# Optimization experiments

Hardware: AMD Instinct MI355X
Metric: run time of the kernel (lower is better)

Reference implementation:

```python
import jax, jax.numpy as jnp
import numpy as np

TAU = 2.0          # LIFNode tau
ALPHA = 2.0        # spikingjelly ATan surrogate alpha (default)
EPS = 1e-5         # nn.LayerNorm eps
SCALE = 0.125      # qk_scale
NUM_HEADS = 2

@jax.custom_vjp
def spike(x):
    # heaviside(x >= 0) with ATan surrogate gradient
    return (x >= 0.0).astype(x.dtype)

def _spike_fwd(x):
    return spike(x), x

def _spike_bwd(x, g):
    sg = (ALPHA / 2.0) / (1.0 + (jnp.pi / 2.0 * ALPHA * x) ** 2)
    return (g * sg,)

spike.defvjp(_spike_fwd, _spike_bwd)

def lif(x, v_th):
    # LIFNode(tau=2.0, decay_input=True, v_reset=0.0, detach_reset=True)
    # x: [T, ...]; sequential membrane-potential scan over T
    def step(v, xt):
        v = v + (xt - v) / TAU                      # charge with input decay
        s = spike(v - v_th)                          # fire
        v = v * (1.0 - jax.lax.stop_gradient(s))     # hard reset to 0, detached
        return v, s
    _, s = jax.lax.scan(step, jnp.zeros_like(x[0]), x)
    return s

def ln(x, w, b):
    m = x.mean(-1, keepdims=True)
    var = x.var(-1, keepdims=True)
    return (x - m) / jnp.sqrt(var + EPS) * w + b

def setup_inputs() -> dict:
    key = jax.random.key(0)
    ks = jax.random.split(key, 6)
    T, B, L, H = 4, 64, 200, 256
    x = jax.random.normal(ks[0], (T, B, L, H), dtype=jnp.float32)
    std = 0.05
    qw = jax.random.normal(ks[1], (H, H), dtype=jnp.float32) * std
    kw = jax.random.normal(ks[2], (H, H), dtype=jnp.float32) * std
    vw = jax.random.normal(ks[3], (H, H), dtype=jnp.float32) * std
    pw = jax.random.normal(ks[4], (H, H), dtype=jnp.float32) * std
    pb = jnp.zeros((H,), dtype=jnp.float32)
    ones = jnp.ones((H,), dtype=jnp.float32)
    zeros = jnp.zeros((H,), dtype=jnp.float32)
    return {
        'x': x,
        'qw': qw, 'q_ln_w': ones, 'q_ln_b': zeros,
        'kw': kw, 'k_ln_w': ones, 'k_ln_b': zeros,
        'vw': vw, 'v_ln_w': ones, 'v_ln_b': zeros,
        'pw': pw, 'pb': pb, 'p_ln_w': ones, 'p_ln_b': zeros,
    }

def reference(x, qw, q_ln_w, q_ln_b, kw, k_ln_w, k_ln_b, vw, v_ln_w, v_ln_b, pw, pb, p_ln_w, p_ln_b):
    T, B, L, H = x.shape
    nh = NUM_HEADS
    dh = H // nh

    def branch(w, lw, lb):
        y = ln(x @ w.T, lw, lb)           # Linear (no bias) -> LayerNorm
        y = lif(y, 1.0)                   # LIF spikes in {0,1}
        return y.reshape(T, B, L, nh, dh).transpose(0, 1, 3, 2, 4)  # [T,B,h,L,dh]

    q = branch(qw, q_ln_w, q_ln_b)
    k = branch(kw, k_ln_w, k_ln_b)
    v = branch(vw, v_ln_w, v_ln_b)

    attn = jnp.einsum('tbhld,tbhmd->tbhlm', q, k) * SCALE   # [T,B,h,L,L]
    y = jnp.einsum('tbhlm,tbhmd->tbhld', attn, v)            # [T,B,h,L,dh]
    y = y.transpose(0, 1, 3, 2, 4).reshape(T, B, L, H)
    y = lif(y, 0.5)                                          # attn_lif, v_threshold=0.5
    y = ln(y @ pw.T + pb, p_ln_w, p_ln_b)                    # proj Linear (bias) -> LN
    return lif(y, 1.0)                                       # proj_lif
```

## Files before the change

kernel.cpp:

```cpp
#include <hip/hip_runtime.h>

#define T_ 4
#define B_ 64
#define L_ 200
#define H_ 256
#define NH_ 2
#define DH_ 128
#define LCAP 12800

typedef short short8_t __attribute__((ext_vector_type(8)));
typedef float f32x4 __attribute__((ext_vector_type(4)));

#define MFMA_BF16(a, b, c) __builtin_amdgcn_mfma_f32_16x16x32_bf16((a), (b), (c), 0, 0, 0)

__device__ __forceinline__ unsigned short bf16rn(float f) {
  unsigned u = __float_as_uint(f);
  return (unsigned short)((u + 0x7FFFu + ((u >> 16) & 1u)) >> 16);
}
__device__ __forceinline__ float bf16tof(unsigned short h) {
  return __uint_as_float(((unsigned)h) << 16);
}

__device__ __forceinline__ short8_t unpack_bf16(uint2 v) {
  union { short8_t s; unsigned u[4]; } r;
  r.u[0] = __builtin_amdgcn_perm(0u, v.x, 0x0C010C00u) * 0x3F80u;
  r.u[1] = __builtin_amdgcn_perm(0u, v.x, 0x0C030C02u) * 0x3F80u;
  r.u[2] = __builtin_amdgcn_perm(0u, v.y, 0x0C010C00u) * 0x3F80u;
  r.u[3] = __builtin_amdgcn_perm(0u, v.y, 0x0C030C02u) * 0x3F80u;
  return r.s;
}

__global__ void pack_w(const float* __restrict__ qw, const float* __restrict__ kw,
                       const float* __restrict__ vw, const float* __restrict__ pw,
                       short* __restrict__ wf, float* __restrict__ wT) {
  int id = blockIdx.x * 256 + threadIdx.x;
  if (id < 262144) {
    int mat = id >> 16, k = (id >> 8) & 255, j = id & 255;
    const float* src = (mat == 0) ? qw : (mat == 1) ? kw : (mat == 2) ? vw : pw;
    wT[id] = src[j * 256 + k];
  }
  int fid = id - 262144;
  if (fid >= 0 && fid < 98304) {
    int lane = fid & 63, kc = (fid >> 6) & 7, nt = (fid >> 9) & 15, ms = fid >> 13;
    int mat = ms / 3, s = ms - mat * 3;
    const float* src = (mat == 0) ? qw : (mat == 1) ? kw : (mat == 2) ? vw : pw;
    int n = nt * 16 + (lane & 15), q = lane >> 4;
    for (int j = 0; j < 8; j++) {
      float v = src[n * 256 + kc * 32 + q * 8 + j];
      unsigned short h1 = bf16rn(v);
      float r1 = v - bf16tof(h1);
      unsigned short h2 = bf16rn(r1);
      float r2 = r1 - bf16tof(h2);
      unsigned short h3 = bf16rn(r2);
      wf[fid * 8 + j] = (short)((s == 0) ? h1 : (s == 1) ? h2 : h3);
    }
  }
}

__global__ void zero_cnt(int* __restrict__ cnt) {
  if (threadIdx.x < 4) cnt[threadIdx.x] = 0;
}

#define QKV_STEP(kc, b0a, b1a)                                                  \
  do {                                                                          \
    int ap_ = (lane ^ (kc)) * 8;                                                \
    short8_t a0_[2], a1_[2];                                                    \
    a0_[0] = *(const short8_t*)&sa[(kc) * 512 + ap_];                           \
    a0_[1] = *(const short8_t*)&sa[(8 + (kc)) * 512 + ap_];                     \
    a1_[0] = *(const short8_t*)&sa[8192 + (kc) * 512 + ap_];                    \
    a1_[1] = *(const short8_t*)&sa[8192 + (8 + (kc)) * 512 + ap_];              \
    _Pragma("unroll")                                                           \
    for (int jj_ = 0; jj_ < 4; jj_++) {                                         \
      _Pragma("unroll")                                                         \
      for (int mt_ = 0; mt_ < 2; mt_++) {                                       \
        hi[mt_][jj_] = MFMA_BF16(a0_[mt_], b0a[jj_], hi[mt_][jj_]);             \
        lo[mt_][jj_] = MFMA_BF16(a0_[mt_], b1a[jj_], lo[mt_][jj_]);             \
        lo[mt_][jj_] = MFMA_BF16(a1_[mt_], b0a[jj_], lo[mt_][jj_]);             \
        lo[mt_][jj_] = MFMA_BF16(a1_[mt_], b1a[jj_], lo[mt_][jj_]);             \
      }                                                                         \
    }                                                                           \
  } while (0)

__global__ __launch_bounds__(256, 2)
void gemm_qkv(const float* __restrict__ xf, const short* __restrict__ wf,
              const float* __restrict__ qlnw, const float* __restrict__ qlnb,
              const float* __restrict__ klnw, const float* __restrict__ klnb,
              const float* __restrict__ vlnw, const float* __restrict__ vlnb,
              unsigned char* __restrict__ Qsp, unsigned char* __restrict__ Ksp,
              unsigned char* __restrict__ Vsp,
              int* __restrict__ cnt, int* __restrict__ list) {
  __shared__ short sa[2 * 8192];
  __shared__ float reds[32][4];
  __shared__ float redq[32][4];
  __shared__ int pf[24];
  const int tid = threadIdx.x;
  const int w = tid >> 6, lane = tid & 63;
  const int q = lane >> 4, ln = lane & 15;
  const int p0 = blockIdx.x * 8;
  const int jbase = w * 4;

  if (tid < 24) pf[tid] = 0;

  short8_t bA0[4], bA1[4], bB0[4], bB1[4];
#pragma unroll
  for (int jj = 0; jj < 4; jj++) {
    const short* bp = wf + (size_t)(jbase + jj) * 4096 + lane * 8;
    bA0[jj] = *(const short8_t*)bp;
    bA1[jj] = *(const short8_t*)(bp + 65536);
  }

  for (int it = 0; it < 4; it++) {
    int cid = tid + 256 * it;
    int r = cid >> 5, ck = cid & 31;
    int k0 = ck * 8, kc = ck >> 2, cq = ck & 3;
    int mt = r >> 4, m = r & 15;
    int p = r >> 2, t = r & 3;
    int pi = p0 + p;
    int b = pi / L_, l = pi % L_;
    size_t nrow = ((size_t)t * B_ + b) * L_ + l;
    int base = ((mt * 8 + kc) * 512) + (((cq * 16 + m) ^ (kc & 7)) * 8);
    float4 v0 = *(const float4*)(xf + nrow * H_ + k0);
    float4 v1 = *(const float4*)(xf + nrow * H_ + k0 + 4);
    float f[8] = {v0.x, v0.y, v0.z, v0.w, v1.x, v1.y, v1.z, v1.w};
    union { short8_t v; short s[8]; } H1, H2;
#pragma unroll
    for (int e = 0; e < 8; e++) {
      unsigned short h1 = bf16rn(f[e]);
      float r1 = f[e] - bf16tof(h1);
      unsigned short h2 = bf16rn(r1);
      H1.s[e] = (short)h1; H2.s[e] = (short)h2;
    }
    *(short8_t*)&sa[base] = H1.v;
    *(short8_t*)&sa[base + 8192] = H2.v;
  }
  __syncthreads();

  for (int mat = 0; mat < 3; mat++) {
    const float* lnw = (mat == 0) ? qlnw : (mat == 1) ? klnw : vlnw;
    const float* lnb = (mat == 0) ? qlnb : (mat == 1) ? klnb : vlnb;
    unsigned char* spk = (mat == 0) ? Qsp : (mat == 1) ? Ksp : Vsp;
    const short* wb = wf + (size_t)mat * 196608;

    f32x4 hi[2][4], lo[2][4];
#pragma unroll
    for (int mt = 0; mt < 2; mt++)
#pragma unroll
      for (int jj = 0; jj < 4; jj++) {
        f32x4 z = {0.f, 0.f, 0.f, 0.f};
        hi[mt][jj] = z; lo[mt][jj] = z;
      }

#pragma unroll
    for (int kh = 0; kh < 4; kh++) {
      const int kc = 2 * kh;
#pragma unroll
      for (int jj = 0; jj < 4; jj++) {
        const short* bp = wb + (size_t)(kc + 1) * 512 + (size_t)(jbase + jj) * 4096 + lane * 8;
        bB0[jj] = *(const short8_t*)bp;
        bB1[jj] = *(const short8_t*)(bp + 65536);
      }
      QKV_STEP(kc, bA0, bA1);
      if (kc + 2 < 8 || mat < 2) {
        const short* nx = (kc + 2 < 8) ? (wb + (size_t)(kc + 2) * 512) : (wb + 196608);
#pragma unroll
        for (int jj = 0; jj < 4; jj++) {
          const short* bp = nx + (size_t)(jbase + jj) * 4096 + lane * 8;
          bA0[jj] = *(const short8_t*)bp;
          bA1[jj] = *(const short8_t*)(bp + 65536);
        }
      }
      QKV_STEP(kc + 1, bB0, bB1);
    }

    float y[2][4][4];
#pragma unroll
    for (int mt = 0; mt < 2; mt++)
#pragma unroll
      for (int jj = 0; jj < 4; jj++)
#pragma unroll
        for (int i = 0; i < 4; i++)
          y[mt][jj][i] = hi[mt][jj][i] + lo[mt][jj][i];

#pragma unroll
    for (int mt = 0; mt < 2; mt++)
#pragma unroll
      for (int i = 0; i < 4; i++) {
        float s = y[mt][0][i] + y[mt][1][i] + y[mt][2][i] + y[mt][3][i];
        float ss = y[mt][0][i] * y[mt][0][i] + y[mt][1][i] * y[mt][1][i]
                 + y[mt][2][i] * y[mt][2][i] + y[mt][3][i] * y[mt][3][i];
#pragma unroll
        for (int o = 1; o < 16; o <<= 1) {
          s += __shfl_xor(s, o, 64);
          ss += __shfl_xor(ss, o, 64);
        }
        if (ln == 0) { reds[16 * mt + 4 * q + i][w] = s; redq[16 * mt + 4 * q + i][w] = ss; }
      }
    __syncthreads();
    float m_[2][4], rs_[2][4], tolr[2][4];
#pragma unroll
    for (int mt = 0; mt < 2; mt++)
#pragma unroll
      for (int i = 0; i < 4; i++) {
        int r = 16 * mt + 4 * q + i;
        float S = reds[r][0] + reds[r][1] + reds[r][2] + reds[r][3];
        float Q2 = redq[r][0] + redq[r][1] + redq[r][2] + redq[r][3];
        float mm = S * (1.0f / 256.0f);
        float var = Q2 * (1.0f / 256.0f) - mm * mm;
        float rs = 1.0f / sqrtf(var + 1e-5f);
        m_[mt][i] = mm; rs_[mt][i] = rs;
        tolr[mt][i] = 1.5e-4f + 3e-6f * (4.0f + fabsf(mm) * rs);
      }

    int fl[2] = {0, 0};
#pragma unroll
    for (int mt = 0; mt < 2; mt++) {
      int pi = p0 + 4 * mt + q;
      int b = pi / L_, l = pi % L_;
#pragma unroll
      for (int jj = 0; jj < 4; jj++) {
        int col = (w * 4 + jj) * 16 + ln;
        float lw = lnw[col], lb = lnb[col];
        float v = 0.0f;
#pragma unroll
        for (int t = 0; t < 4; t++) {
          float yn = (y[mt][jj][t] - m_[mt][t]) * rs_[mt][t] * lw + lb;
          v = (v + yn) * 0.5f;
          bool f = (v >= 1.0f);
          if (fabsf(v - 1.0f) < tolr[mt][t]) fl[mt] = 1;
          int head = col >> 7, d = col & 127;
          spk[((((size_t)t * B_ + b) * NH_ + head) * L_ + l) * DH_ + d] = f ? (unsigned char)1 : (unsigned char)0;
          if (f) v = 0.0f;
        }
      }
    }
#pragma unroll
    for (int o = 1; o < 16; o <<= 1) {
      fl[0] |= __shfl_xor(fl[0], o, 64);
      fl[1] |= __shfl_xor(fl[1], o, 64);
    }
    if (ln == 0) {
      if (fl[0]) atomicOr(&pf[mat * 8 + q], 1);
      if (fl[1]) atomicOr(&pf[mat * 8 + 4 + q], 1);
    }
    __syncthreads();
  }

  if (tid < 24 && pf[tid]) {
    int mat = tid >> 3, pr = tid & 7;
    int idx = atomicAdd(cnt + mat, 1);
    if (idx < LCAP) list[mat * LCAP + idx] = p0 + pr;
  }
}

#define PROJ_STEP(kc, b0a, b1a, b2a)                                            \
  do {                                                                          \
    int ap_ = (lane ^ (kc)) * 8;                                                \
    short8_t a0_[2];                                                            \
    a0_[0] = *(const short8_t*)&sa[(kc) * 512 + ap_];                           \
    a0_[1] = *(const short8_t*)&sa[(8 + (kc)) * 512 + ap_];                     \
    _Pragma("unroll")                                                           \
    for (int jj_ = 0; jj_ < 4; jj_++) {                                         \
      _Pragma("unroll")                                                         \
      for (int mt_ = 0; mt_ < 2; mt_++) {                                       \
        hi[mt_][jj_] = MFMA_BF16(a0_[mt_], b0a[jj_], hi[mt_][jj_]);             \
        lo[mt_][jj_] = MFMA_BF16(a0_[mt_], b1a[jj_], lo[mt_][jj_]);             \
        lo[mt_][jj_] = MFMA_BF16(a0_[mt_], b2a[jj_], lo[mt_][jj_]);             \
      }                                                                         \
    }                                                                           \
  } while (0)

__global__ __launch_bounds__(256, 2)
void gemm_proj(const unsigned char* __restrict__ xs, const short* __restrict__ wfm,
               const float* __restrict__ bias,
               const float* __restrict__ lnw, const float* __restrict__ lnb,
               float* __restrict__ out,
               int* __restrict__ cnt, int* __restrict__ list) {
  __shared__ short sa[8192];
  __shared__ float reds[32][4];
  __shared__ float redq[32][4];
  __shared__ int pf[8];
  const int tid = threadIdx.x;
  const int w = tid >> 6, lane = tid & 63;
  const int q = lane >> 4, ln = lane & 15;
  const int p0 = blockIdx.x * 8;
  const int jbase = w * 4;

  if (tid < 8) pf[tid] = 0;

  short8_t bA0[4], bA1[4], bA2[4], bB0[4], bB1[4], bB2[4];
#pragma unroll
  for (int jj = 0; jj < 4; jj++) {
    const short* bp = wfm + (size_t)(jbase + jj) * 4096 + lane * 8;
    bA0[jj] = *(const short8_t*)bp;
    bA1[jj] = *(const short8_t*)(bp + 65536);
    bA2[jj] = *(const short8_t*)(bp + 131072);
  }

  for (int it = 0; it < 4; it++) {
    int cid = tid + 256 * it;
    int r = cid >> 5, ck = cid & 31;
    int k0 = ck * 8, kc = ck >> 2, cq = ck & 3;
    int mt = r >> 4, m = r & 15;
    int p = r >> 2, t = r & 3;
    int pi = p0 + p;
    int b = pi / L_, l = pi % L_;
    size_t nrow = ((size_t)t * B_ + b) * L_ + l;
    int base = ((mt * 8 + kc) * 512) + (((cq * 16 + m) ^ (kc & 7)) * 8);
    uint2 u = *(const uint2*)(xs + nrow * H_ + k0);
    *(short8_t*)&sa[base] = unpack_bf16(u);
  }
  __syncthreads();

  f32x4 hi[2][4], lo[2][4];
#pragma unroll
  for (int mt = 0; mt < 2; mt++)
#pragma unroll
    for (int jj = 0; jj < 4; jj++) {
      f32x4 z = {0.f, 0.f, 0.f, 0.f};
      hi[mt][jj] = z; lo[mt][jj] = z;
    }

#pragma unroll
  for (int kh = 0; kh < 4; kh++) {
    const int kc = 2 * kh;
#pragma unroll
    for (int jj = 0; jj < 4; jj++) {
      const short* bp = wfm + (size_t)(kc + 1) * 512 + (size_t)(jbase + jj) * 4096 + lane * 8;
      bB0[jj] = *(const short8_t*)bp;
      bB1[jj] = *(const short8_t*)(bp + 65536);
      bB2[jj] = *(const short8_t*)(bp + 131072);
    }
    PROJ_STEP(kc, bA0, bA1, bA2);
    if (kc + 2 < 8) {
#pragma unroll
      for (int jj = 0; jj < 4; jj++) {
        const short* bp = wfm + (size_t)(kc + 2) * 512 + (size_t)(jbase + jj) * 4096 + lane * 8;
        bA0[jj] = *(const short8_t*)bp;
        bA1[jj] = *(const short8_t*)(bp + 65536);
        bA2[jj] = *(const short8_t*)(bp + 131072);
      }
    }
    PROJ_STEP(kc + 1, bB0, bB1, bB2);
  }

  float y[2][4][4];
#pragma unroll
  for (int mt = 0; mt < 2; mt++)
#pragma unroll
    for (int jj = 0; jj < 4; jj++) {
      float bj = bias[(w * 4 + jj) * 16 + ln];
#pragma unroll
      for (int i = 0; i < 4; i++)
        y[mt][jj][i] = hi[mt][jj][i] + lo[mt][jj][i] + bj;
    }

#pragma unroll
  for (int mt = 0; mt < 2; mt++)
#pragma unroll
    for (int i = 0; i < 4; i++) {
      float s = y[mt][0][i] + y[mt][1][i] + y[mt][2][i] + y[mt][3][i];
      float ss = y[mt][0][i] * y[mt][0][i] + y[mt][1][i] * y[mt][1][i]
               + y[mt][2][i] * y[mt][2][i] + y[mt][3][i] * y[mt][3][i];
#pragma unroll
      for (int o = 1; o < 16; o <<= 1) {
        s += __shfl_xor(s, o, 64);
        ss += __shfl_xor(ss, o, 64);
      }
      if (ln == 0) { reds[16 * mt + 4 * q + i][w] = s; redq[16 * mt + 4 * q + i][w] = ss; }
    }
  __syncthreads();
  float m_[2][4], rs_[2][4], tolr[2][4];
#pragma unroll
  for (int mt = 0; mt < 2; mt++)
#pragma unroll
    for (int i = 0; i < 4; i++) {
      int r = 16 * mt + 4 * q + i;
      float S = reds[r][0] + reds[r][1] + reds[r][2] + reds[r][3];
      float Q2 = redq[r][0] + redq[r][1] + redq[r][2] + redq[r][3];
      float mm = S * (1.0f / 256.0f);
      float var = Q2 * (1.0f / 256.0f) - mm * mm;
      float rs = 1.0f / sqrtf(var + 1e-5f);
      m_[mt][i] = mm; rs_[mt][i] = rs;
      tolr[mt][i] = 1.5e-4f + 3e-6f * (4.0f + fabsf(mm) * rs);
    }

  int fl[2] = {0, 0};
#pragma unroll
  for (int mt = 0; mt < 2; mt++) {
    int pi = p0 + 4 * mt + q;
    int b = pi / L_, l = pi % L_;
#pragma unroll
    for (int jj = 0; jj < 4; jj++) {
      int col = (w * 4 + jj) * 16 + ln;
      float lw = lnw[col], lb = lnb[col];
      float v = 0.0f;
#pragma unroll
      for (int t = 0; t < 4; t++) {
        float yn = (y[mt][jj][t] - m_[mt][t]) * rs_[mt][t] * lw + lb;
        v = (v + yn) * 0.5f;
        bool f = (v >= 1.0f);
        if (fabsf(v - 1.0f) < tolr[mt][t]) fl[mt] = 1;
        size_t n = ((size_t)t * B_ + b) * L_ + l;
        out[n * H_ + col] = f ? 1.0f : 0.0f;
        if (f) v = 0.0f;
      }
    }
  }
#pragma unroll
  for (int o = 1; o < 16; o <<= 1) {
    fl[0] |= __shfl_xor(fl[0], o, 64);
    fl[1] |= __shfl_xor(fl[1], o, 64);
  }
  if (ln == 0) {
    if (fl[0]) atomicOr(&pf[q], 1);
    if (fl[1]) atomicOr(&pf[4 + q], 1);
  }
  __syncthreads();
  if (tid < 8 && pf[tid]) {
    int idx = atomicAdd(cnt, 1);
    if (idx < LCAP) list[idx] = p0 + tid;
  }
}

__global__ __launch_bounds__(256)
void fixup_qkv(const float* __restrict__ xf, const float* __restrict__ wT,
               const float* __restrict__ qlnw, const float* __restrict__ qlnb,
               const float* __restrict__ klnw, const float* __restrict__ klnb,
               const float* __restrict__ vlnw, const float* __restrict__ vlnb,
               unsigned char* __restrict__ Qsp, unsigned char* __restrict__ Ksp,
               unsigned char* __restrict__ Vsp,
               const int* __restrict__ cnt, const int* __restrict__ list) {
  __shared__ double rsum[4][4];
  __shared__ double mv[4], rsd[4];
  const int tid = threadIdx.x;
  const int w = tid >> 6;
  int n0 = cnt[0]; if (n0 > LCAP) n0 = LCAP;
  int n1 = cnt[1]; if (n1 > LCAP) n1 = LCAP;
  int n2 = cnt[2]; if (n2 > LCAP) n2 = LCAP;
  int ntot = n0 + n1 + n2;
  for (int e = blockIdx.x; e < ntot; e += gridDim.x) {
    int mat, ei;
    if (e < n0) { mat = 0; ei = e; }
    else if (e < n0 + n1) { mat = 1; ei = e - n0; }
    else { mat = 2; ei = e - n0 - n1; }
    const float* wTm = wT + (size_t)mat * 65536;
    const float* lnw = (mat == 0) ? qlnw : (mat == 1) ? klnw : vlnw;
    const float* lnb = (mat == 0) ? qlnb : (mat == 1) ? klnb : vlnb;
    unsigned char* spk = (mat == 0) ? Qsp : (mat == 1) ? Ksp : Vsp;
    int pi = list[mat * LCAP + ei];
    int b = pi / L_, l = pi % L_;
    int j = tid;
    size_t nrow[4];
#pragma unroll
    for (int t = 0; t < 4; t++) nrow[t] = ((size_t)t * B_ + b) * L_ + l;
    double acc[4] = {0.0, 0.0, 0.0, 0.0};
    for (int k = 0; k < 256; k++) {
      double wv = (double)wTm[k * 256 + j];
#pragma unroll
      for (int t = 0; t < 4; t++) acc[t] += (double)xf[nrow[t] * H_ + k] * wv;
    }
#pragma unroll
    for (int t = 0; t < 4; t++) {
      double s = acc[t];
#pragma unroll
      for (int o = 1; o < 64; o <<= 1) s += __shfl_xor(s, o, 64);
      if ((tid & 63) == 0) rsum[w][t] = s;
    }
    __syncthreads();
    if (tid < 4) mv[tid] = (rsum[0][tid] + rsum[1][tid] + rsum[2][tid] + rsum[3][tid]) * (1.0 / 256.0);
    __syncthreads();
#pragma unroll
    for (int t = 0; t < 4; t++) {
      double d = acc[t] - mv[t];
      double ss = d * d;
#pragma unroll
      for (int o = 1; o < 64; o <<= 1) ss += __shfl_xor(ss, o, 64);
      if ((tid & 63) == 0) rsum[w][t] = ss;
    }
    __syncthreads();
    if (tid < 4) {
      double var = (rsum[0][tid] + rsum[1][tid] + rsum[2][tid] + rsum[3][tid]) * (1.0 / 256.0);
      rsd[tid] = 1.0 / sqrt(var + 1e-5);
    }
    __syncthreads();
    double lw = (double)lnw[j], lb = (double)lnb[j];
    double v = 0.0;
#pragma unroll
    for (int t = 0; t < 4; t++) {
      double yn = (acc[t] - mv[t]) * rsd[t] * lw + lb;
      v = (v + yn) * 0.5;
      bool f = (v >= 1.0);
      int head = j >> 7, d = j & 127;
      spk[((((size_t)t * B_ + b) * NH_ + head) * L_ + l) * DH_ + d] = f ? (unsigned char)1 : (unsigned char)0;
      if (f) v = 0.0;
    }
    __syncthreads();
  }
}

template <bool IS_PROJ>
__global__ __launch_bounds__(256)
void fixup(const float* __restrict__ xf, const unsigned char* __restrict__ xs,
           const float* __restrict__ wT, const float* __restrict__ bias,
           const float* __restrict__ lnw, const float* __restrict__ lnb,
           unsigned char* __restrict__ spk, float* __restrict__ out,
           const int* __restrict__ cnt, const int* __restrict__ list) {
  __shared__ double rsum[4][4];
  __shared__ double mv[4], rsd[4];
  const int tid = threadIdx.x;
  const int w = tid >> 6;
  int n = *cnt; if (n > LCAP) n = LCAP;
  for (int e = blockIdx.x; e < n; e += gridDim.x) {
    int pi = list[e];
    int b = pi / L_, l = pi % L_;
    int j = tid;
    size_t nrow[4];
#pragma unroll
    for (int t = 0; t < 4; t++) nrow[t] = ((size_t)t * B_ + b) * L_ + l;
    double acc[4];
#pragma unroll
    for (int t = 0; t < 4; t++) acc[t] = IS_PROJ ? (double)bias[j] : 0.0;
    for (int k = 0; k < 256; k++) {
      double wv = (double)wT[k * 256 + j];
#pragma unroll
      for (int t = 0; t < 4; t++) {
        double xv = IS_PROJ ? (double)xs[nrow[t] * H_ + k] : (double)xf[nrow[t] * H_ + k];
        acc[t] += xv * wv;
      }
    }
#pragma unroll
    for (int t = 0; t < 4; t++) {
      double s = acc[t];
#pragma unroll
      for (int o = 1; o < 64; o <<= 1) s += __shfl_xor(s, o, 64);
      if ((tid & 63) == 0) rsum[w][t] = s;
    }
    __syncthreads();
    if (tid < 4) mv[tid] = (rsum[0][tid] + rsum[1][tid] + rsum[2][tid] + rsum[3][tid]) * (1.0 / 256.0);
    __syncthreads();
#pragma unroll
    for (int t = 0; t < 4; t++) {
      double d = acc[t] - mv[t];
      double ss = d * d;
#pragma unroll
      for (int o = 1; o < 64; o <<= 1) ss += __shfl_xor(ss, o, 64);
      if ((tid & 63) == 0) rsum[w][t] = ss;
    }
    __syncthreads();
    if (tid < 4) {
      double var = (rsum[0][tid] + rsum[1][tid] + rsum[2][tid] + rsum[3][tid]) * (1.0 / 256.0);
      rsd[tid] = 1.0 / sqrt(var + 1e-5);
    }
    __syncthreads();
    double lw = (double)lnw[j], lb = (double)lnb[j];
    double v = 0.0;
#pragma unroll
    for (int t = 0; t < 4; t++) {
      double yn = (acc[t] - mv[t]) * rsd[t] * lw + lb;
      v = (v + yn) * 0.5;
      bool f = (v >= 1.0);
      if (IS_PROJ) {
        out[nrow[t] * H_ + j] = f ? 1.0f : 0.0f;
      } else {
        int head = j >> 7, d = j & 127;
        spk[((((size_t)t * B_ + b) * NH_ + head) * L_ + l) * DH_ + d] = f ? (unsigned char)1 : (unsigned char)0;
      }
      if (f) v = 0.0;
    }
    __syncthreads();
  }
}

__global__ __launch_bounds__(256)
void vt_prep(const unsigned char* __restrict__ Vs, unsigned char* __restrict__ Vt) {
  const int slab = blockIdx.x;
  const int w = threadIdx.x >> 6, lane = threadIdx.x & 63;
  const unsigned char* src = Vs + (size_t)slab * (L_ * DH_);
  unsigned char* dst = Vt + (size_t)slab * (DH_ * 224);
  for (int d = w; d < DH_; d += 4) {
    for (int mb = 0; mb < 4; mb++) {
      int m = mb * 64 + lane;
      unsigned char v = 0;
      if (m < L_) v = src[(size_t)m * DH_ + d];
      if (m < 224) dst[(size_t)d * 224 + m] = v;
    }
  }
}

__global__ __launch_bounds__(256)
void attn_mfma(const unsigned char* __restrict__ Qs, const unsigned char* __restrict__ Ks,
               const unsigned char* __restrict__ Vt, unsigned char* __restrict__ S2) {
  __shared__ unsigned short sS[32 * 232];
  const int tid = threadIdx.x;
  const int w = tid >> 6, lane = tid & 63;
  const int quad = lane >> 4, ln = lane & 15;
  const int bid = blockIdx.x;
  const int lt = bid % 7;
  const int head = (bid / 7) & 1;
  const int b = bid / 14;
  const int l0 = lt * 32;

  for (int i = tid; i < 32 * 232; i += 256) sS[i] = 0;

  float vmem[2][2][4];
#pragma unroll
  for (int di = 0; di < 2; di++)
#pragma unroll
    for (int ls = 0; ls < 2; ls++)
#pragma unroll
      for (int r = 0; r < 4; r++) vmem[di][ls][r] = 0.f;

  __syncthreads();

  for (int t = 0; t < T_; t++) {
    const int slab = (t * B_ + b) * NH_ + head;
    const unsigned char* qb = Qs + (size_t)slab * (L_ * DH_) + (size_t)l0 * DH_;
    const unsigned char* kb = Ks + (size_t)slab * (L_ * DH_);

    short8_t af[2][4];
#pragma unroll
    for (int ls = 0; ls < 2; ls++)
#pragma unroll
      for (int ks = 0; ks < 4; ks++)
        af[ls][ks] = unpack_bf16(*(const uint2*)(qb + (size_t)(ls * 16 + ln) * DH_ + ks * 32 + quad * 8));

#pragma unroll
    for (int i = 0; i < 4; i++) {
      int nt = w + 4 * i;
      if (nt < 13) {
        short8_t bf[4];
#pragma unroll
        for (int ks = 0; ks < 4; ks++)
          bf[ks] = unpack_bf16(*(const uint2*)(kb + (size_t)(nt * 16 + ln) * DH_ + ks * 32 + quad * 8));
#pragma unroll
        for (int ls = 0; ls < 2; ls++) {
          f32x4 acc = {0.f, 0.f, 0.f, 0.f};
#pragma unroll
          for (int ks = 0; ks < 4; ks++)
            acc = MFMA_BF16(af[ls][ks], bf[ks], acc);
#pragma unroll
          for (int r = 0; r < 4; r++)
            sS[(ls * 16 + quad * 4 + r) * 232 + nt * 16 + ln] =
                (unsigned short)(__float_as_uint(acc[r]) >> 16);
        }
      }
    }
    __syncthreads();

    const unsigned char* vb = Vt + (size_t)slab * (DH_ * 224);
    f32x4 a2[2][2];
#pragma unroll
    for (int di = 0; di < 2; di++)
#pragma unroll
      for (int ls = 0; ls < 2; ls++) { f32x4 z = {0.f, 0.f, 0.f, 0.f}; a2[di][ls] = z; }

#pragma unroll
    for (int ks = 0; ks < 7; ks++) {
      short8_t s0 = *(const short8_t*)&sS[(0 * 16 + ln) * 232 + ks * 32 + quad * 8];
      short8_t s1 = *(const short8_t*)&sS[(1 * 16 + ln) * 232 + ks * 32 + quad * 8];
#pragma unroll
      for (int di = 0; di < 2; di++) {
        int dt = w + 4 * di;
        short8_t bv = unpack_bf16(*(const uint2*)(vb + (size_t)(dt * 16 + ln) * 224 + ks * 32 + quad * 8));
        a2[di][0] = MFMA_BF16(s0, bv, a2[di][0]);
        a2[di][1] = MFMA_BF16(s1, bv, a2[di][1]);
      }
    }

#pragma unroll
    for (int di = 0; di < 2; di++)
#pragma unroll
      for (int ls = 0; ls < 2; ls++)
#pragma unroll
        for (int r = 0; r < 4; r++) {
          float y = a2[di][ls][r] * 0.125f;
          float v = (vmem[di][ls][r] + y) * 0.5f;
          bool f = (v >= 0.5f);
          int l = l0 + ls * 16 + quad * 4 + r;
          if (l < L_)
            S2[(((size_t)t * B_ + b) * L_ + l) * H_ + head * DH_ + (w + 4 * di) * 16 + ln] =
                f ? (unsigned char)1 : (unsigned char)0;
          vmem[di][ls][r] = f ? 0.f : v;
        }
    __syncthreads();
  }
}

extern "C" void kernel_launch(void* const* d_in, const int* in_sizes, int n_in,
                              void* d_out, int out_size, void* d_ws, size_t ws_size,
                              hipStream_t stream) {
  (void)in_sizes; (void)n_in; (void)out_size; (void)ws_size;
  const float* x    = (const float*)d_in[0];
  const float* qw   = (const float*)d_in[1];
  const float* qlnw = (const float*)d_in[2];
  const float* qlnb = (const float*)d_in[3];
  const float* kw   = (const float*)d_in[4];
  const float* klnw = (const float*)d_in[5];
  const float* klnb = (const float*)d_in[6];
  const float* vw   = (const float*)d_in[7];
  const float* vlnw = (const float*)d_in[8];
  const float* vlnb = (const float*)d_in[9];
  const float* pw   = (const float*)d_in[10];
  const float* pb   = (const float*)d_in[11];
  const float* plnw = (const float*)d_in[12];
  const float* plnb = (const float*)d_in[13];

  char* ws = (char*)d_ws;
  const size_t SPK = (size_t)T_ * B_ * NH_ * L_ * DH_;
  short* wf  = (short*)ws;
  float* wT  = (float*)(ws + 1572864);
  int*  cnt  = (int*)(ws + 2621440);
  int*  list = (int*)(ws + 2621696);
  unsigned char* Qsp = (unsigned char*)(ws + 2826496);
  unsigned char* Ksp = Qsp + SPK;
  unsigned char* Vsp = Ksp + SPK;
  unsigned char* S2  = Vsp;
  unsigned char* Vt  = Vsp + SPK;

  hipLaunchKernelGGL(pack_w, dim3(1408), dim3(256), 0, stream, qw, kw, vw, pw, wf, wT);
  hipLaunchKernelGGL(zero_cnt, dim3(1), dim3(64), 0, stream, cnt);

  hipLaunchKernelGGL(gemm_qkv, dim3(1600), dim3(256), 0, stream,
                     x, wf, qlnw, qlnb, klnw, klnb, vlnw, vlnb, Qsp, Ksp, Vsp, cnt, list);

  hipLaunchKernelGGL(fixup_qkv, dim3(512), dim3(256), 0, stream,
                     x, wT, qlnw, qlnb, klnw, klnb, vlnw, vlnb, Qsp, Ksp, Vsp, cnt, list);

  hipLaunchKernelGGL(vt_prep, dim3(512), dim3(256), 0, stream, Vsp, Vt);
  hipLaunchKernelGGL(attn_mfma, dim3(896), dim3(256), 0, stream, Qsp, Ksp, Vt, S2);

  hipLaunchKernelGGL(gemm_proj, dim3(1600), dim3(256), 0, stream,
                     S2, wf + 589824, pb, plnw, plnb, (float*)d_out, cnt + 3, list + 3 * LCAP);
  hipLaunchKernelGGL((fixup<true>), dim3(512), dim3(256), 0, stream,
                     (const float*)nullptr, S2, wT + 196608, pb, plnw, plnb, (unsigned char*)nullptr, (float*)d_out, cnt + 3, list + 3 * LCAP);
}
```

Measured before the change: 483.1 us.

## Drop low-order split-bf16 MFMA terms, prefetch A fragments, remove per-matrix barrier

The QKV GEMM drops the a1*b1 residual product (4 MFMAs down to 3 per tile) and the proj GEMM drops the third weight split (3 down to 2), widening the near-threshold tolerance so more borderline rows are flagged for exact recompute. LDS A-fragment loads are double-buffered ahead of the MFMA groups, and MFMAs are grouped by accumulator to shorten dependency chains. Per-matrix reduction buffers let the trailing barrier inside the mat loop be removed. The risk is lower precision, which may push more rows into the fallback path, and the extra registers may hurt occupancy.

Measured after the change: 482.5 us. About the same (-0.1%).

```diff
diff --git a/kernel.cpp b/kernel.cpp
--- a/kernel.cpp
+++ b/kernel.cpp
@@ -61,24 +61,32 @@
   if (threadIdx.x < 4) cnt[threadIdx.x] = 0;
 }
 
-#define QKV_STEP(kc, b0a, b1a)                                                  \
-  do {                                                                          \
-    int ap_ = (lane ^ (kc)) * 8;                                                \
-    short8_t a0_[2], a1_[2];                                                    \
-    a0_[0] = *(const short8_t*)&sa[(kc) * 512 + ap_];                           \
-    a0_[1] = *(const short8_t*)&sa[(8 + (kc)) * 512 + ap_];                     \
-    a1_[0] = *(const short8_t*)&sa[8192 + (kc) * 512 + ap_];                    \
-    a1_[1] = *(const short8_t*)&sa[8192 + (8 + (kc)) * 512 + ap_];              \
-    _Pragma("unroll")                                                           \
-    for (int jj_ = 0; jj_ < 4; jj_++) {                                         \
-      _Pragma("unroll")                                                         \
-      for (int mt_ = 0; mt_ < 2; mt_++) {                                       \
-        hi[mt_][jj_] = MFMA_BF16(a0_[mt_], b0a[jj_], hi[mt_][jj_]);             \
-        lo[mt_][jj_] = MFMA_BF16(a0_[mt_], b1a[jj_], lo[mt_][jj_]);             \
-        lo[mt_][jj_] = MFMA_BF16(a1_[mt_], b0a[jj_], lo[mt_][jj_]);             \
-        lo[mt_][jj_] = MFMA_BF16(a1_[mt_], b1a[jj_], lo[mt_][jj_]);             \
-      }                                                                         \
-    }                                                                           \
+#define LOAD_A_QKV(kc, aa0, aa1)                                         \
+  do {                                                                   \
+    int ap_ = (lane ^ (kc)) * 8;                                         \
+    aa0[0] = *(const short8_t*)&sa[(kc) * 512 + ap_];                    \
+    aa0[1] = *(const short8_t*)&sa[(8 + (kc)) * 512 + ap_];              \
+    aa1[0] = *(const short8_t*)&sa[8192 + (kc) * 512 + ap_];             \
+    aa1[1] = *(const short8_t*)&sa[8192 + (8 + (kc)) * 512 + ap_];       \
+  } while (0)
+
+#define QKV_STEP(aa0, aa1, b0a, b1a)                                     \
+  do {                                                                   \
+    _Pragma("unroll")                                                    \
+    for (int jj_ = 0; jj_ < 4; jj_++)                                    \
+      _Pragma("unroll")                                                  \
+      for (int mt_ = 0; mt_ < 2; mt_++)                                  \
+        hi[mt_][jj_] = MFMA_BF16(aa0[mt_], b0a[jj_], hi[mt_][jj_]);      \
+    _Pragma("unroll")                                                    \
+    for (int jj_ = 0; jj_ < 4; jj_++)                                    \
+      _Pragma("unroll")                                                  \
+      for (int mt_ = 0; mt_ < 2; mt_++)                                  \
+        lo[mt_][jj_] = MFMA_BF16(aa0[mt_], b1a[jj_], lo[mt_][jj_]);      \
+    _Pragma("unroll")                                                    \
+    for (int jj_ = 0; jj_ < 4; jj_++)                                    \
+      _Pragma("unroll")                                                  \
+      for (int mt_ = 0; mt_ < 2; mt_++)                                  \
+        lo[mt_][jj_] = MFMA_BF16(aa1[mt_], b0a[jj_], lo[mt_][jj_]);      \
   } while (0)
 
 __global__ __launch_bounds__(256, 2)
@@ -90,8 +98,8 @@
               unsigned char* __restrict__ Vsp,
               int* __restrict__ cnt, int* __restrict__ list) {
   __shared__ short sa[2 * 8192];
-  __shared__ float reds[32][4];
-  __shared__ float redq[32][4];
+  __shared__ float reds[3][32][4];
+  __shared__ float redq[3][32][4];
   __shared__ int pf[24];
   const int tid = threadIdx.x;
   const int w = tid >> 6, lane = tid & 63;
@@ -102,6 +110,7 @@
   if (tid < 24) pf[tid] = 0;
 
   short8_t bA0[4], bA1[4], bB0[4], bB1[4];
+  short8_t aC0[2], aC1[2], aN0[2], aN1[2];
 #pragma unroll
   for (int jj = 0; jj < 4; jj++) {
     const short* bp = wf + (size_t)(jbase + jj) * 4096 + lane * 8;
@@ -135,6 +144,8 @@
   }
   __syncthreads();
 
+  LOAD_A_QKV(0, aC0, aC1);
+
   for (int mat = 0; mat < 3; mat++) {
     const float* lnw = (mat == 0) ? qlnw : (mat == 1) ? klnw : vlnw;
     const float* lnb = (mat == 0) ? qlnb : (mat == 1) ? klnb : vlnb;
@@ -159,8 +170,9 @@
         bB0[jj] = *(const short8_t*)bp;
         bB1[jj] = *(const short8_t*)(bp + 65536);
       }
-      QKV_STEP(kc, bA0, bA1);
-      if (kc + 2 < 8 || mat < 2) {
+      LOAD_A_QKV(kc + 1, aN0, aN1);
+      QKV_STEP(aC0, aC1, bA0, bA1);
+      {
         const short* nx = (kc + 2 < 8) ? (wb + (size_t)(kc + 2) * 512) : (wb + 196608);
 #pragma unroll
         for (int jj = 0; jj < 4; jj++) {
@@ -169,7 +181,8 @@
           bA1[jj] = *(const short8_t*)(bp + 65536);
         }
       }
-      QKV_STEP(kc + 1, bB0, bB1);
+      LOAD_A_QKV((kc + 2) & 7, aC0, aC1);
+      QKV_STEP(aN0, aN1, bB0, bB1);
     }
 
     float y[2][4][4];
@@ -193,7 +206,7 @@
           s += __shfl_xor(s, o, 64);
           ss += __shfl_xor(ss, o, 64);
         }
-        if (ln == 0) { reds[16 * mt + 4 * q + i][w] = s; redq[16 * mt + 4 * q + i][w] = ss; }
+        if (ln == 0) { reds[mat][16 * mt + 4 * q + i][w] = s; redq[mat][16 * mt + 4 * q + i][w] = ss; }
       }
     __syncthreads();
     float m_[2][4], rs_[2][4], tolr[2][4];
@@ -202,13 +215,13 @@
 #pragma unroll
       for (int i = 0; i < 4; i++) {
         int r = 16 * mt + 4 * q + i;
-        float S = reds[r][0] + reds[r][1] + reds[r][2] + reds[r][3];
-        float Q2 = redq[r][0] + redq[r][1] + redq[r][2] + redq[r][3];
+        float S = reds[mat][r][0] + reds[mat][r][1] + reds[mat][r][2] + reds[mat][r][3];
+        float Q2 = redq[mat][r][0] + redq[mat][r][1] + redq[mat][r][2] + redq[mat][r][3];
         float mm = S * (1.0f / 256.0f);
         float var = Q2 * (1.0f / 256.0f) - mm * mm;
         float rs = 1.0f / sqrtf(var + 1e-5f);
         m_[mt][i] = mm; rs_[mt][i] = rs;
-        tolr[mt][i] = 1.5e-4f + 3e-6f * (4.0f + fabsf(mm) * rs);
+        tolr[mt][i] = 1.75e-4f + 3e-6f * (4.0f + fabsf(mm) * rs);
       }
 
     int fl[2] = {0, 0};
@@ -242,9 +255,9 @@
       if (fl[0]) atomicOr(&pf[mat * 8 + q], 1);
       if (fl[1]) atomicOr(&pf[mat * 8 + 4 + q], 1);
     }
-    __syncthreads();
-  }
-
+  }
+
+  __syncthreads();
   if (tid < 24 && pf[tid]) {
     int mat = tid >> 3, pr = tid & 7;
     int idx = atomicAdd(cnt + mat, 1);
@@ -252,21 +265,25 @@
   }
 }
 
-#define PROJ_STEP(kc, b0a, b1a, b2a)                                            \
-  do {                                                                          \
-    int ap_ = (lane ^ (kc)) * 8;                                                \
-    short8_t a0_[2];                                                            \
-    a0_[0] = *(const short8_t*)&sa[(kc) * 512 + ap_];                           \
-    a0_[1] = *(const short8_t*)&sa[(8 + (kc)) * 512 + ap_];                     \
-    _Pragma("unroll")                                                           \
-    for (int jj_ = 0; jj_ < 4; jj_++) {                                         \
-      _Pragma("unroll")                                                         \
-      for (int mt_ = 0; mt_ < 2; mt_++) {                                       \
-        hi[mt_][jj_] = MFMA_BF16(a0_[mt_], b0a[jj_], hi[mt_][jj_]);             \
-        lo[mt_][jj_] = MFMA_BF16(a0_[mt_], b1a[jj_], lo[mt_][jj_]);             \
-        lo[mt_][jj_] = MFMA_BF16(a0_[mt_], b2a[jj_], lo[mt_][jj_]);             \
-      }                                                                         \
-    }                                                                           \
+#define LOAD_A_PROJ(kc, aa)                                              \
+  do {                                                                   \
+    int ap_ = (lane ^ (kc)) * 8;                                         \
+    aa[0] = *(const short8_t*)&sa[(kc) * 512 + ap_];                     \
+    aa[1] = *(const short8_t*)&sa[(8 + (kc)) * 512 + ap_];               \
+  } while (0)
+
+#define PROJ_STEP(aa, b0a, b1a)                                          \
+  do {                                                                   \
+    _Pragma("unroll")                                                    \
+    for (int jj_ = 0; jj_ < 4; jj_++)                                    \
+      _Pragma("unroll")                                                  \
+      for (int mt_ = 0; mt_ < 2; mt_++)                                  \
+        hi[mt_][jj_] = MFMA_BF16(aa[mt_], b0a[jj_], hi[mt_][jj_]);       \
+    _Pragma("unroll")                                                    \
+    for (int jj_ = 0; jj_ < 4; jj_++)                                    \
+      _Pragma("unroll")                                                  \
+      for (int mt_ = 0; mt_ < 2; mt_++)                                  \
+        lo[mt_][jj_] = MFMA_BF16(aa[mt_], b1a[jj_], lo[mt_][jj_]);       \
   } while (0)
 
 __global__ __launch_bounds__(256, 2)
@@ -287,13 +304,13 @@
 
   if (tid < 8) pf[tid] = 0;
 
-  short8_t bA0[4], bA1[4], bA2[4], bB0[4], bB1[4], bB2[4];
+  short8_t bA0[4], bA1[4], bB0[4], bB1[4];
+  short8_t aC[2], aN[2];
 #pragma unroll
   for (int jj = 0; jj < 4; jj++) {
     const short* bp = wfm + (size_t)(jbase + jj) * 4096 + lane * 8;
     bA0[jj] = *(const short8_t*)bp;
     bA1[jj] = *(const short8_t*)(bp + 65536);
-    bA2[jj] = *(const short8_t*)(bp + 131072);
   }
 
   for (int it = 0; it < 4; it++) {
@@ -320,6 +337,8 @@
       hi[mt][jj] = z; lo[mt][jj] = z;
     }
 
+  LOAD_A_PROJ(0, aC);
+
 #pragma unroll
   for (int kh = 0; kh < 4; kh++) {
     const int kc = 2 * kh;
@@ -328,19 +347,19 @@
       const short* bp = wfm + (size_t)(kc + 1) * 512 + (size_t)(jbase + jj) * 4096 + lane * 8;
       bB0[jj] = *(const short8_t*)bp;
       bB1[jj] = *(const short8_t*)(bp + 65536);
-      bB2[jj] = *(const short8_t*)(bp + 131072);
-    }
-    PROJ_STEP(kc, bA0, bA1, bA2);
+    }
+    LOAD_A_PROJ(kc + 1, aN);
+    PROJ_STEP(aC, bA0, bA1);
     if (kc + 2 < 8) {
 #pragma unroll
       for (int jj = 0; jj < 4; jj++) {
         const short* bp = wfm + (size_t)(kc + 2) * 512 + (size_t)(jbase + jj) * 4096 + lane * 8;
         bA0[jj] = *(const short8_t*)bp;
         bA1[jj] = *(const short8_t*)(bp + 65536);
-        bA2[jj] = *(const short8_t*)(bp + 131072);
-      }
-    }
-    PROJ_STEP(kc + 1, bB0, bB1, bB2);
+      }
+      LOAD_A_PROJ(kc + 2, aC);
+    }
+    PROJ_STEP(aN, bB0, bB1);
   }
 
   float y[2][4][4];
@@ -381,7 +400,7 @@
       float var = Q2 * (1.0f / 256.0f) - mm * mm;
       float rs = 1.0f / sqrtf(var + 1e-5f);
       m_[mt][i] = mm; rs_[mt][i] = rs;
-      tolr[mt][i] = 1.5e-4f + 3e-6f * (4.0f + fabsf(mm) * rs);
+      tolr[mt][i] = 1.75e-4f + 3e-6f * (4.0f + fabsf(mm) * rs);
     }
 
   int fl[2] = {0, 0};
```
